# Performance work log

Hardware: AMD Instinct MI355X
Metric: run time of the kernel (lower is better)

Reference implementation:

```python
import jax, jax.numpy as jnp
import numpy as np
from functools import partial

NUM_CLASSES = 4
HEAD_OUTS = [4, 2, 1, 3, 2, 2]  # class, offset, z, size, yaw, vel -> sum 14
VOXEL = (0.1, 0.1)
PC_RANGE = (0.0, -39.68, -3.0, 100.0, 39.68, 1.0)
MIN_RADIUS = 2.0
BN_EPS = 1e-5


def setup_inputs() -> dict:
    key = jax.random.key(0)
    ks = jax.random.split(key, 12)
    B, C, H, W, N = 4, 256, 200, 200, 128
    spatial_features = jax.random.normal(ks[0], (B, C, H, W), jnp.float32)
    # gt boxes: x,y,z,w,l,h,yaw,cls,vx,vy ; coords chosen so grid idx in [0,200)
    x = jax.random.uniform(ks[1], (B, N), jnp.float32, 0.5, 19.5)
    y = jax.random.uniform(ks[2], (B, N), jnp.float32, -39.0, -20.0)
    z = jax.random.uniform(ks[3], (B, N), jnp.float32, -2.0, 0.0)
    dims = jax.random.uniform(ks[4], (B, N, 3), jnp.float32, 1.0, 4.0)
    yaw = jax.random.uniform(ks[5], (B, N), jnp.float32, -3.14159, 3.14159)
    cls = jax.random.randint(ks[6], (B, N), 0, NUM_CLASSES).astype(jnp.float32)
    vel = 0.1 * jax.random.normal(ks[7], (B, N, 2), jnp.float32)
    gt = jnp.concatenate([x[..., None], y[..., None], z[..., None], dims,
                          yaw[..., None], cls[..., None], vel], axis=-1)
    # zero out last 16 boxes per sample -> filtered by validity mask
    gt = gt.at[:, -16:, :].set(0.0)
    w1 = 0.05 * jax.random.normal(ks[8], (6, C, C, 3, 3), jnp.float32)
    bn_gamma = jnp.ones((6, C), jnp.float32)
    bn_beta = jnp.zeros((6, C), jnp.float32)
    bn_mean = 0.1 * jax.random.normal(ks[9], (6, C), jnp.float32)
    bn_var = jax.random.uniform(ks[10], (6, C), jnp.float32, 0.5, 1.5)
    w2 = 0.05 * jax.random.normal(ks[11], (14, C, 1, 1), jnp.float32)
    b2 = jnp.zeros((14,), jnp.float32)
    return {"spatial_features": spatial_features, "gt_boxes": gt, "w1": w1,
            "bn_gamma": bn_gamma, "bn_beta": bn_beta, "bn_mean": bn_mean,
            "bn_var": bn_var, "w2": w2, "b2": b2}


def _conv(x, w, pad):
    return jax.lax.conv_general_dilated(x, w, (1, 1), pad,
                                        dimension_numbers=("NCHW", "OIHW", "NCHW"))


def _heads(x, w1, g, b, m, v, w2, b2):
    outs, o = [], 0
    for i, nout in enumerate(HEAD_OUTS):
        h = _conv(x, w1[i], "SAME")  # [B,C,H,W]
        h = g[i][None, :, None, None] * (h - m[i][None, :, None, None]) \
            * jax.lax.rsqrt(v[i][None, :, None, None] + BN_EPS) + b[i][None, :, None, None]
        h = jax.nn.relu(h)
        outs.append(_conv(h, w2[o:o + nout], "VALID") + b2[o:o + nout][None, :, None, None])
        o += nout
    return jnp.concatenate(outs, axis=1)  # [B,14,H,W]


def _targets(gt, H, W):
    B, N = gt.shape[:2]
    x, y, z = gt[..., 0], gt[..., 1], gt[..., 2]
    bw, bl, bh = gt[..., 3], gt[..., 4], gt[..., 5]
    yaw = gt[..., 6]
    cls = jnp.clip(gt[..., 7].astype(jnp.int32), 0, NUM_CLASSES - 1)
    vel = gt[..., 8:10]
    valid = (jnp.abs(x) + jnp.abs(y) + jnp.abs(z)) > 0
    gx = (x - PC_RANGE[0]) / VOXEL[0]
    gy = (y - PC_RANGE[1]) / VOXEL[1]
    gxi = jnp.floor(gx).astype(jnp.int32)
    gyi = jnp.floor(gy).astype(jnp.int32)
    valid = valid & (gxi >= 0) & (gxi < W) & (gyi >= 0) & (gyi < H)
    xoff = gx - gxi.astype(gx.dtype)
    yoff = gy - gyi.astype(gy.dtype)
    # scalar targets scatter (invalid boxes dropped via out-of-range flat index)
    vals = jnp.stack([xoff, yoff, z, bw, bl, bh, jnp.sin(yaw), jnp.cos(yaw),
                      vel[..., 0], vel[..., 1], jnp.ones_like(x)], axis=-1)  # [B,N,11]
    bidx = jnp.broadcast_to(jnp.arange(B, dtype=jnp.int32)[:, None], (B, N))
    flat = bidx * (H * W) + gyi * W + gxi
    flat = jnp.where(valid, flat, B * H * W)  # out of range -> dropped
    scat = jnp.zeros((B * H * W, 11), jnp.float32)
    scat = scat.at[flat.reshape(-1)].set(vals.reshape(-1, 11), mode="drop")
    scalars = scat.reshape(B, H, W, 11).transpose(0, 3, 1, 2)  # [B,11,H,W]
    # gaussian heatmap: per-box splat, scatter-max into class channel
    sigma = jnp.maximum(jnp.sqrt(bw ** 2 + bl ** 2) / 2.0, MIN_RADIUS) / 3.0  # [B,N]
    xs = jnp.arange(W, dtype=jnp.float32)
    ys = jnp.arange(H, dtype=jnp.float32)
    d2 = (xs[None, None, None, :] - gxi[..., None, None].astype(jnp.float32)) ** 2 + \
         (ys[None, None, :, None] - gyi[..., None, None].astype(jnp.float32)) ** 2  # [B,N,H,W]
    gauss = jnp.exp(-d2 / (2.0 * sigma[..., None, None] ** 2))
    gauss = jnp.where(valid[..., None, None], gauss, 0.0)
    heat = jnp.zeros((B, NUM_CLASSES, H, W), jnp.float32)
    heat = heat.at[bidx, cls].max(gauss)
    return jnp.concatenate([heat, scalars], axis=1)  # [B,15,H,W]


def reference(spatial_features, gt_boxes, w1, bn_gamma, bn_beta, bn_mean, bn_var, w2, b2):
    H, W = spatial_features.shape[-2:]
    preds = _heads(spatial_features, w1, bn_gamma, bn_beta, bn_mean, bn_var, w2, b2)
    tgts = _targets(gt_boxes, H, W)
    return jnp.concatenate([preds, tgts], axis=1)  # [B,29,H,W]
```

## Files before the change

### kernel.cpp

```cpp
#include <hip/hip_runtime.h>

typedef __attribute__((ext_vector_type(8))) short short8;
typedef __attribute__((ext_vector_type(4))) float f32x4;
typedef __attribute__((ext_vector_type(4))) unsigned short us4;
typedef __attribute__((ext_vector_type(8))) unsigned short us8;

union FragU { short8 s; us4 h[2]; us8 u; };

__device__ __forceinline__ unsigned short f2bf(float f) {
  union { float f; unsigned int u; } v; v.f = f;
  unsigned int r = (v.u + 0x7fffu + ((v.u >> 16) & 1u)) >> 16;
  return (unsigned short)r;
}

typedef const __attribute__((address_space(1))) unsigned int* gas1_t;
typedef __attribute__((address_space(3))) unsigned int* las3_t;
__device__ __forceinline__ void glds16(const void* g, void* l) {
  __builtin_amdgcn_global_load_lds((gas1_t)g, (las3_t)l, 16, 0, 0);
}

__global__ void transpose_pad_k(const float* __restrict__ sf, unsigned short* __restrict__ Xtp) {
  __shared__ float tile[32][33];
  int b = blockIdx.z, c0 = blockIdx.y * 32, p0 = blockIdx.x * 32;
  int tx = threadIdx.x, ty = threadIdx.y;
#pragma unroll
  for (int i = 0; i < 4; ++i)
    tile[ty + i * 8][tx] = sf[((size_t)(b * 256 + c0 + ty + i * 8) * 40000) + p0 + tx];
  __syncthreads();
#pragma unroll
  for (int i = 0; i < 4; ++i) {
    int p = p0 + ty + i * 8;
    int y = p / 200, x = p - y * 200;
    size_t pf = (size_t)b * 40804 + (size_t)(y + 1) * 202 + (x + 1);
    Xtp[(pf << 8) + c0 + tx] = f2bf(tile[tx][ty + i * 8]);
  }
}

__global__ void border_zero_k(unsigned short* __restrict__ Xtp) {
  int t = blockIdx.x * 256 + threadIdx.x;
  if (t >= 4 * 804 * 32) return;
  int ch8 = t & 31;
  int rest = t >> 5;
  int p = rest % 804, b = rest / 804;
  int y, x;
  if (p < 202)      { y = 0;           x = p; }
  else if (p < 404) { y = 201;         x = p - 202; }
  else if (p < 604) { y = p - 404 + 1; x = 0; }
  else              { y = p - 604 + 1; x = 201; }
  size_t pf = (size_t)b * 40804 + (size_t)y * 202 + x;
  *(us8*)&Xtp[(pf << 8) + ch8 * 8] = (us8){0, 0, 0, 0, 0, 0, 0, 0};
}

__global__ void prep_w1f_k(const float* __restrict__ w1, const float* __restrict__ gamma,
                           const float* __restrict__ var, unsigned short* __restrict__ W1f) {
  int id = blockIdx.x * 256 + threadIdx.x;
  if (id >= 6 * 256 * 2304) return;
  int k = id % 2304;
  int rest = id / 2304;
  int oc = rest & 255, h = rest >> 8;
  int tap = k >> 8, c = k & 255;
  int hc = h * 256 + oc;
  float s = gamma[hc] * rsqrtf(var[hc] + 1e-5f);
  W1f[id] = f2bf(s * w1[(hc * 256 + c) * 9 + tap]);
}

__global__ __launch_bounds__(256, 2) void conv_head_v6_k(
    const unsigned short* __restrict__ Xtp, const unsigned short* __restrict__ W1f,
    const float* __restrict__ gamma, const float* __restrict__ beta,
    const float* __restrict__ mean, const float* __restrict__ var,
    const float* __restrict__ w2, const float* __restrict__ b2,
    float* __restrict__ out) {
  const int NOUT[6] = {4, 2, 1, 3, 2, 2};
  const int OFFS[6] = {0, 4, 6, 7, 10, 12};
  __shared__ __align__(16) char smem[73728];
  unsigned short* h_s = (unsigned short*)smem;

  int tid = threadIdx.x;
  int head = blockIdx.z, b = blockIdx.y;
  int p_loc = blockIdx.x * 128;
  int nout = NOUT[head], ooff = OFFS[head];

  int wid = tid >> 6, lane = tid & 63;
  int wm = wid >> 1, wn = wid & 1;
  int l15 = lane & 15, lhi = lane >> 4;

  int r0 = tid >> 2;
  int cbsw = (((tid & 3) ^ ((tid >> 3) & 3)) << 4);
  int pA0 = p_loc + r0;       if (pA0 > 39999) pA0 = 39999;
  int pA1 = p_loc + r0 + 64;  if (pA1 > 39999) pA1 = 39999;
  int ay0 = pA0 / 200, ax0 = pA0 - ay0 * 200;
  int ay1 = pA1 / 200, ax1 = pA1 - ay1 * 200;
  const char* xb = (const char*)Xtp + (size_t)b * 40804 * 512;
  const char* As0 = xb + (size_t)((ay0 + 1) * 202 + ax0 + 1) * 512 + cbsw;
  const char* As1 = xb + (size_t)((ay1 + 1) * 202 + ax1 + 1) * 512 + cbsw;

  const char* Bs0 = (const char*)W1f + (size_t)(head * 256 + r0) * 4608 + cbsw;
  const char* Bs1 = Bs0 + (size_t)64 * 4608;
  const char* Bs2 = Bs0 + (size_t)128 * 4608;
  const char* Bs3 = Bs0 + (size_t)192 * 4608;

  char* rA = smem;
  char* rB = smem + 24576;
  char* rC = smem + 49152;

  auto STAGE = [&](int kn, char* dst) {
    int tap = kn >> 3;
    int c0b = (kn & 7) << 6;
    int t3 = tap / 3;
    int doff = (t3 - 1) * 202 + (tap - t3 * 3 - 1);
    long ab = (long)doff * 512 + c0b;
    long bb = (long)kn * 64;
    glds16(As0 + ab, dst + wid * 1024);
    glds16(As1 + ab, dst + wid * 1024 + 4096);
    glds16(Bs0 + bb, dst + 8192 + wid * 1024);
    glds16(Bs1 + bb, dst + 8192 + wid * 1024 + 4096);
    glds16(Bs2 + bb, dst + 8192 + wid * 1024 + 8192);
    glds16(Bs3 + bb, dst + 8192 + wid * 1024 + 12288);
  };

  f32x4 acc[4][8];
#pragma unroll
  for (int mi = 0; mi < 4; ++mi)
#pragma unroll
    for (int ni = 0; ni < 8; ++ni) acc[mi][ni] = (f32x4){0.f, 0.f, 0.f, 0.f};

  STAGE(0, rA);
  STAGE(1, rB);

  int slotA = (lhi ^ ((l15 >> 1) & 3)) * 8;

  for (int kt = 0; kt < 72; ++kt) {
    if (kt < 71) asm volatile("s_waitcnt vmcnt(6)" ::: "memory");
    else         asm volatile("s_waitcnt vmcnt(0)" ::: "memory");
    __builtin_amdgcn_sched_barrier(0);
    __builtin_amdgcn_s_barrier();
    __builtin_amdgcn_sched_barrier(0);

    if (kt < 70) STAGE(kt + 2, rC);

    const unsigned short* A_sh = (const unsigned short*)rA;
    const unsigned short* B_sh = (const unsigned short*)(rA + 8192);
    short8 af[4], bfr[8];
#pragma unroll
    for (int mi = 0; mi < 4; ++mi) {
      FragU u;
      u.u = *(const us8*)&A_sh[(wm * 64 + mi * 16 + l15) * 32 + slotA];
      af[mi] = u.s;
    }
#pragma unroll
    for (int ni = 0; ni < 8; ++ni) {
      FragU u;
      u.u = *(const us8*)&B_sh[(wn * 128 + ni * 16 + l15) * 32 + slotA];
      bfr[ni] = u.s;
    }
    __builtin_amdgcn_s_setprio(1);
#pragma unroll
    for (int mi = 0; mi < 4; ++mi)
#pragma unroll
      for (int ni = 0; ni < 8; ++ni)
        acc[mi][ni] = __builtin_amdgcn_mfma_f32_16x16x32_bf16(af[mi], bfr[ni], acc[mi][ni], 0, 0, 0);
    __builtin_amdgcn_s_setprio(0);

    char* t = rA; rA = rB; rB = rC; rC = t;
  }

  {
    float tbr[8];
#pragma unroll
    for (int ni = 0; ni < 8; ++ni) {
      int hc = head * 256 + wn * 128 + ni * 16 + l15;
      float s = gamma[hc] * rsqrtf(var[hc] + 1e-5f);
      tbr[ni] = beta[hc] - s * mean[hc];
    }
#pragma unroll
    for (int mi = 0; mi < 4; ++mi)
#pragma unroll
      for (int ni = 0; ni < 8; ++ni)
#pragma unroll
        for (int r = 0; r < 4; ++r)
          acc[mi][ni][r] = fmaxf(acc[mi][ni][r] + tbr[ni], 0.f);
  }
  short8 wfr[8];
  {
    int jr = (l15 < nout) ? (ooff + l15) : 0;
    const float* wrow = w2 + jr * 256;
#pragma unroll
    for (int kc = 0; kc < 8; ++kc) {
      int koff = kc * 32 + lhi * 8;
      FragU u;
#pragma unroll
      for (int q = 0; q < 8; ++q) u.u[q] = f2bf(wrow[koff + q]);
      wfr[kc] = u.s;
    }
  }
  __syncthreads();
#pragma unroll
  for (int mi = 0; mi < 4; ++mi) {
#pragma unroll
    for (int ni = 0; ni < 8; ++ni) {
      int ocl = wn * 128 + ni * 16 + l15;
#pragma unroll
      for (int r = 0; r < 4; ++r) {
        int px = wm * 64 + mi * 16 + lhi * 4 + r;
        h_s[px * 264 + ocl] = f2bf(acc[mi][ni][r]);
      }
    }
  }
  __syncthreads();

#pragma unroll
  for (int g2 = 0; g2 < 2; ++g2) {
    int grp = wid * 2 + g2;
    float b2v = (l15 < nout) ? b2[ooff + l15] : 0.f;
    f32x4 oacc = (f32x4){0.f, 0.f, 0.f, 0.f};
#pragma unroll
    for (int kc = 0; kc < 8; ++kc) {
      int koff = kc * 32 + lhi * 8;
      FragU hu;
      hu.u = *(const us8*)&h_s[(grp * 16 + l15) * 264 + koff];
      oacc = __builtin_amdgcn_mfma_f32_16x16x32_bf16(hu.s, wfr[kc], oacc, 0, 0, 0);
    }
    if (l15 < nout) {
      float* dst = out + (size_t)(b * 29 + ooff + l15) * 40000;
#pragma unroll
      for (int r = 0; r < 4; ++r) {
        int px_g = p_loc + grp * 16 + lhi * 4 + r;
        if (px_g < 40000) dst[px_g] = oacc[r] + b2v;
      }
    }
  }
}

__global__ __launch_bounds__(512) void conv_head_nows_k(
    const float* __restrict__ sf, const float* __restrict__ w1,
    const float* __restrict__ gamma, const float* __restrict__ beta,
    const float* __restrict__ mean, const float* __restrict__ var,
    const float* __restrict__ w2, const float* __restrict__ b2,
    float* __restrict__ out) {
  const int NOUT[6] = {4, 2, 1, 3, 2, 2};
  const int OFFS[6] = {0, 4, 6, 7, 10, 12};
  __shared__ __align__(16) char smem[78080];
  unsigned short* A_s  = (unsigned short*)smem;
  unsigned short* B_s  = (unsigned short*)(smem + 9216);
  unsigned short* h_s  = (unsigned short*)smem;
  unsigned short* w2_s = (unsigned short*)(smem + 67584);
  float* tb_s          = (float*)(smem + 76032);
  float* s_s           = (float*)(smem + 77056);

  int tid = threadIdx.x;
  int head = blockIdx.z, b = blockIdx.y;
  int p_loc = blockIdx.x * 128;
  int nout = NOUT[head], ooff = OFFS[head];
  {
    int j = tid >> 5, c8 = (tid & 31) * 8;
    us8 t;
#pragma unroll
    for (int q = 0; q < 8; ++q)
      t[q] = (j < nout) ? f2bf(w2[(ooff + j) * 256 + c8 + q]) : (unsigned short)0;
    *(us8*)&w2_s[j * 264 + c8] = t;
  }
  if (tid < 256) {
    int hc = head * 256 + tid;
    float s = gamma[hc] * rsqrtf(var[hc] + 1e-5f);
    s_s[tid] = s;
    tb_s[tid] = beta[hc] - s * mean[hc];
  }
  __syncthreads();

  int wid = tid >> 6, lane = tid & 63;
  int wm = wid >> 2, wn = wid & 3;
  int l15 = lane & 15, lhi = lane >> 4;
  int cg = wid, mm = lane;
  int p0 = p_loc + mm, p1 = p0 + 64;
  int ay0 = p0 / 200, ax0 = p0 - ay0 * 200;
  int ay1 = p1 / 200, ax1 = p1 - ay1 * 200;
  const float* sfb = sf + (size_t)b * 256 * 40000;
  int oc = tid >> 1, half = tid & 1;
  const float* w1h = w1 + ((size_t)head * 256 + oc) * 2304;
  float sv = s_s[oc];

  f32x4 acc[4][4];
#pragma unroll
  for (int mi = 0; mi < 4; ++mi)
#pragma unroll
    for (int ni = 0; ni < 4; ++ni) acc[mi][ni] = (f32x4){0.f, 0.f, 0.f, 0.f};

  for (int kt = 0; kt < 72; ++kt) {
    int tap = kt >> 3;
    int c0 = (kt & 7) << 5;
    int t3 = tap / 3;
    int dy = t3 - 1, dx = tap - t3 * 3 - 1;
    {
      const float* src = sfb + (size_t)(c0 + cg * 4) * 40000;
      int yy = ay0 + dy, xx = ax0 + dx;
      us4 v = (us4){0, 0, 0, 0};
      if ((unsigned)yy < 200u && (unsigned)xx < 200u) {
        int pix = yy * 200 + xx;
        v[0] = f2bf(src[pix]);
        v[1] = f2bf(src[40000 + pix]);
        v[2] = f2bf(src[80000 + pix]);
        v[3] = f2bf(src[120000 + pix]);
      }
      *(us4*)&A_s[mm * 36 + cg * 4] = v;
      yy = ay1 + dy; xx = ax1 + dx;
      us4 w = (us4){0, 0, 0, 0};
      if ((unsigned)yy < 200u && (unsigned)xx < 200u) {
        int pix = yy * 200 + xx;
        w[0] = f2bf(src[pix]);
        w[1] = f2bf(src[40000 + pix]);
        w[2] = f2bf(src[80000 + pix]);
        w[3] = f2bf(src[120000 + pix]);
      }
      *(us4*)&A_s[(mm + 64) * 36 + cg * 4] = w;
    }
    {
      int kk = half * 16;
#pragma unroll
      for (int g = 0; g < 4; ++g) {
        us4 t;
#pragma unroll
        for (int q = 0; q < 4; ++q)
          t[q] = f2bf(sv * w1h[(c0 + kk + g * 4 + q) * 9 + tap]);
        *(us4*)&B_s[oc * 36 + kk + g * 4] = t;
      }
    }
    __syncthreads();
    short8 af[4], bfr[4];
#pragma unroll
    for (int mi = 0; mi < 4; ++mi) {
      int a = (wm * 64 + mi * 16 + l15) * 36 + lhi * 8;
      FragU u;
      u.h[0] = *(const us4*)&A_s[a];
      u.h[1] = *(const us4*)&A_s[a + 4];
      af[mi] = u.s;
    }
#pragma unroll
    for (int ni = 0; ni < 4; ++ni) {
      int a = (wn * 64 + ni * 16 + l15) * 36 + lhi * 8;
      FragU u;
      u.h[0] = *(const us4*)&B_s[a];
      u.h[1] = *(const us4*)&B_s[a + 4];
      bfr[ni] = u.s;
    }
#pragma unroll
    for (int mi = 0; mi < 4; ++mi)
#pragma unroll
      for (int ni = 0; ni < 4; ++ni)
        acc[mi][ni] = __builtin_amdgcn_mfma_f32_16x16x32_bf16(af[mi], bfr[ni], acc[mi][ni], 0, 0, 0);
    __syncthreads();
  }
#pragma unroll
  for (int mi = 0; mi < 4; ++mi) {
#pragma unroll
    for (int ni = 0; ni < 4; ++ni) {
      int ocl = wn * 64 + ni * 16 + l15;
      float tbv = tb_s[ocl];
#pragma unroll
      for (int r = 0; r < 4; ++r) {
        int px = wm * 64 + mi * 16 + lhi * 4 + r;
        float v = fmaxf(acc[mi][ni][r] + tbv, 0.f);
        h_s[px * 264 + ocl] = f2bf(v);
      }
    }
  }
  __syncthreads();
  {
    int j = l15;
    float b2v = (j < nout) ? b2[ooff + j] : 0.f;
    f32x4 oacc = (f32x4){0.f, 0.f, 0.f, 0.f};
#pragma unroll
    for (int kc = 0; kc < 8; ++kc) {
      int koff = kc * 32 + lhi * 8;
      FragU hu, wu;
      hu.u = *(const us8*)&h_s[(wid * 16 + l15) * 264 + koff];
      wu.u = *(const us8*)&w2_s[l15 * 264 + koff];
      oacc = __builtin_amdgcn_mfma_f32_16x16x32_bf16(hu.s, wu.s, oacc, 0, 0, 0);
    }
    if (j < nout) {
      float* dst = out + (size_t)(b * 29 + ooff + j) * 40000;
#pragma unroll
      for (int r = 0; r < 4; ++r) {
        int px_g = p_loc + wid * 16 + lhi * 4 + r;
        if (px_g < 40000) dst[px_g] = oacc[r] + b2v;
      }
    }
  }
}

__global__ void heat_k(const float* __restrict__ gt, float* __restrict__ out) {
  __shared__ float bx[128], by[128], binv[128];
  __shared__ int bcls[128];
  int b = blockIdx.y, tid = threadIdx.x;
  if (tid < 128) {
    const float* g = gt + (b * 128 + tid) * 10;
    float x = g[0], y = g[1], z = g[2];
    bool valid = fabsf(x) + fabsf(y) + fabsf(z) > 0.f;
    float gx = x / 0.1f;
    float gy = (y + 39.68f) / 0.1f;
    float fx = floorf(gx), fy = floorf(gy);
    int gxi = (int)fx, gyi = (int)fy;
    valid = valid && gxi >= 0 && gxi < 200 && gyi >= 0 && gyi < 200;
    float bw = g[3], bl = g[4];
    float sigma = fmaxf(sqrtf(bw * bw + bl * bl) * 0.5f, 2.0f) / 3.0f;
    binv[tid] = valid ? 1.f / (2.f * sigma * sigma) : -1.f;
    bx[tid] = fx;
    by[tid] = fy;
    bcls[tid] = min(max((int)g[7], 0), 3);
  }
  __syncthreads();
  int pid = blockIdx.x * 256 + tid;
  if (pid >= 40000) return;
  float py = (float)(pid / 200);
  float px = (float)(pid - (pid / 200) * 200);
  float h0 = 0.f, h1 = 0.f, h2 = 0.f, h3 = 0.f;
  for (int n = 0; n < 128; ++n) {
    float inv = binv[n];
    if (inv < 0.f) continue;
    float ddx = px - bx[n], ddy = py - by[n];
    float t = (ddx * ddx + ddy * ddy) * inv;
    if (t > 40.f) continue;
    float e = __expf(-t);
    int c = bcls[n];
    h0 = fmaxf(h0, c == 0 ? e : 0.f);
    h1 = fmaxf(h1, c == 1 ? e : 0.f);
    h2 = fmaxf(h2, c == 2 ? e : 0.f);
    h3 = fmaxf(h3, c == 3 ? e : 0.f);
  }
  int base = (b * 29 + 14) * 40000 + pid;
  out[base] = h0;
  out[base + 40000] = h1;
  out[base + 80000] = h2;
  out[base + 120000] = h3;
#pragma unroll
  for (int q = 0; q < 11; ++q) out[base + (4 + q) * 40000] = 0.f;
}

__global__ void scatter_k(const float* __restrict__ gt, float* __restrict__ out) {
  int b = threadIdx.x;
  if (b >= 4) return;
  for (int n = 0; n < 128; ++n) {
    const float* g = gt + (b * 128 + n) * 10;
    float x = g[0], y = g[1], z = g[2];
    if (!(fabsf(x) + fabsf(y) + fabsf(z) > 0.f)) continue;
    float gx = x / 0.1f;
    float gy = (y + 39.68f) / 0.1f;
    float fx = floorf(gx), fy = floorf(gy);
    int gxi = (int)fx, gyi = (int)fy;
    if (gxi < 0 || gxi >= 200 || gyi < 0 || gyi >= 200) continue;
    int base = (b * 29 + 18) * 40000 + gyi * 200 + gxi;
    out[base] = gx - fx;
    out[base + 1 * 40000] = gy - fy;
    out[base + 2 * 40000] = z;
    out[base + 3 * 40000] = g[3];
    out[base + 4 * 40000] = g[4];
    out[base + 5 * 40000] = g[5];
    out[base + 6 * 40000] = sinf(g[6]);
    out[base + 7 * 40000] = cosf(g[6]);
    out[base + 8 * 40000] = g[8];
    out[base + 9 * 40000] = g[9];
    out[base + 10 * 40000] = 1.f;
  }
}

extern "C" void kernel_launch(void* const* d_in, const int* in_sizes, int n_in,
                              void* d_out, int out_size, void* d_ws, size_t ws_size,
                              hipStream_t stream) {
  const float* sf    = (const float*)d_in[0];
  const float* gt    = (const float*)d_in[1];
  const float* w1    = (const float*)d_in[2];
  const float* gamma = (const float*)d_in[3];
  const float* beta  = (const float*)d_in[4];
  const float* mean  = (const float*)d_in[5];
  const float* var   = (const float*)d_in[6];
  const float* w2    = (const float*)d_in[7];
  const float* b2    = (const float*)d_in[8];
  float* out = (float*)d_out;
  char* ws = (char*)d_ws;

  const size_t W1F_BYTES = (size_t)6 * 256 * 2304 * 2;
  const size_t XTP_BYTES = (size_t)4 * 40804 * 256 * 2;
  unsigned short* W1f = (unsigned short*)ws;

  dim3 cgrid(313, 4, 6);
  if (ws_size >= W1F_BYTES + XTP_BYTES) {
    unsigned short* Xtp = (unsigned short*)(ws + W1F_BYTES);
    prep_w1f_k<<<(6 * 256 * 2304 + 255) / 256, 256, 0, stream>>>(w1, gamma, var, W1f);
    border_zero_k<<<(4 * 804 * 32 + 255) / 256, 256, 0, stream>>>(Xtp);
    transpose_pad_k<<<dim3(1250, 8, 4), dim3(32, 8), 0, stream>>>(sf, Xtp);
    conv_head_v6_k<<<cgrid, 256, 0, stream>>>(Xtp, W1f, gamma, beta, mean, var, w2, b2, out);
  } else {
    conv_head_nows_k<<<cgrid, 512, 0, stream>>>(sf, w1, gamma, beta, mean, var, w2, b2, out);
  }
  heat_k<<<dim3(157, 4), 256, 0, stream>>>(gt, out);
  scatter_k<<<1, 64, 0, stream>>>(gt, out);
}
```

Baseline: 1.211 ms.

## Switch conv head to double-buffered staging and fp32 scalar 1x1 epilogue

```diff
diff --git a/kernel.cpp b/kernel.cpp
--- a/kernel.cpp
+++ b/kernel.cpp
@@ -64,7 +64,7 @@
   W1f[id] = f2bf(s * w1[(hc * 256 + c) * 9 + tap]);
 }
 
-__global__ __launch_bounds__(256, 2) void conv_head_v6_k(
+__global__ __launch_bounds__(256, 2) void conv_head_v9_k(
     const unsigned short* __restrict__ Xtp, const unsigned short* __restrict__ W1f,
     const float* __restrict__ gamma, const float* __restrict__ beta,
     const float* __restrict__ mean, const float* __restrict__ var,
@@ -72,8 +72,7 @@
     float* __restrict__ out) {
   const int NOUT[6] = {4, 2, 1, 3, 2, 2};
   const int OFFS[6] = {0, 4, 6, 7, 10, 12};
-  __shared__ __align__(16) char smem[73728];
-  unsigned short* h_s = (unsigned short*)smem;
+  __shared__ __align__(16) char smem[49152];
 
   int tid = threadIdx.x;
   int head = blockIdx.z, b = blockIdx.y;
@@ -101,7 +100,6 @@
 
   char* rA = smem;
   char* rB = smem + 24576;
-  char* rC = smem + 49152;
 
   auto STAGE = [&](int kn, char* dst) {
     int tap = kn >> 3;
@@ -125,18 +123,16 @@
     for (int ni = 0; ni < 8; ++ni) acc[mi][ni] = (f32x4){0.f, 0.f, 0.f, 0.f};
 
   STAGE(0, rA);
-  STAGE(1, rB);
 
   int slotA = (lhi ^ ((l15 >> 1) & 3)) * 8;
 
   for (int kt = 0; kt < 72; ++kt) {
-    if (kt < 71) asm volatile("s_waitcnt vmcnt(6)" ::: "memory");
-    else         asm volatile("s_waitcnt vmcnt(0)" ::: "memory");
+    asm volatile("s_waitcnt vmcnt(0)" ::: "memory");
     __builtin_amdgcn_sched_barrier(0);
     __builtin_amdgcn_s_barrier();
     __builtin_amdgcn_sched_barrier(0);
 
-    if (kt < 70) STAGE(kt + 2, rC);
+    if (kt < 71) STAGE(kt + 1, rB);
 
     const unsigned short* A_sh = (const unsigned short*)rA;
     const unsigned short* B_sh = (const unsigned short*)(rA + 8192);
@@ -161,7 +157,7 @@
         acc[mi][ni] = __builtin_amdgcn_mfma_f32_16x16x32_bf16(af[mi], bfr[ni], acc[mi][ni], 0, 0, 0);
     __builtin_amdgcn_s_setprio(0);
 
-    char* t = rA; rA = rB; rB = rC; rC = t;
+    char* t = rA; rA = rB; rB = t;
   }
 
   {
@@ -180,52 +176,48 @@
         for (int r = 0; r < 4; ++r)
           acc[mi][ni][r] = fmaxf(acc[mi][ni][r] + tbr[ni], 0.f);
   }
-  short8 wfr[8];
-  {
-    int jr = (l15 < nout) ? (ooff + l15) : 0;
-    const float* wrow = w2 + jr * 256;
-#pragma unroll
-    for (int kc = 0; kc < 8; ++kc) {
-      int koff = kc * 32 + lhi * 8;
-      FragU u;
-#pragma unroll
-      for (int q = 0; q < 8; ++q) u.u[q] = f2bf(wrow[koff + q]);
-      wfr[kc] = u.s;
-    }
-  }
-  __syncthreads();
-#pragma unroll
-  for (int mi = 0; mi < 4; ++mi) {
-#pragma unroll
-    for (int ni = 0; ni < 8; ++ni) {
-      int ocl = wn * 128 + ni * 16 + l15;
-#pragma unroll
-      for (int r = 0; r < 4; ++r) {
-        int px = wm * 64 + mi * 16 + lhi * 4 + r;
-        h_s[px * 264 + ocl] = f2bf(acc[mi][ni][r]);
-      }
-    }
-  }
-  __syncthreads();
-
-#pragma unroll
-  for (int g2 = 0; g2 < 2; ++g2) {
-    int grp = wid * 2 + g2;
-    float b2v = (l15 < nout) ? b2[ooff + l15] : 0.f;
-    f32x4 oacc = (f32x4){0.f, 0.f, 0.f, 0.f};
-#pragma unroll
-    for (int kc = 0; kc < 8; ++kc) {
-      int koff = kc * 32 + lhi * 8;
-      FragU hu;
-      hu.u = *(const us8*)&h_s[(grp * 16 + l15) * 264 + koff];
-      oacc = __builtin_amdgcn_mfma_f32_16x16x32_bf16(hu.s, wfr[kc], oacc, 0, 0, 0);
-    }
-    if (l15 < nout) {
-      float* dst = out + (size_t)(b * 29 + ooff + l15) * 40000;
-#pragma unroll
-      for (int r = 0; r < 4; ++r) {
-        int px_g = p_loc + grp * 16 + lhi * 4 + r;
-        if (px_g < 40000) dst[px_g] = oacc[r] + b2v;
+
+  float* hcs = (float*)smem;
+#pragma unroll
+  for (int chunk = 0; chunk < 4; ++chunk) {
+    __syncthreads();
+    if (wm == (chunk >> 1)) {
+      int mi0 = (chunk & 1) * 2;
+#pragma unroll
+      for (int mi2 = 0; mi2 < 2; ++mi2) {
+#pragma unroll
+        for (int ni = 0; ni < 8; ++ni) {
+          int ocl = wn * 128 + ni * 16 + l15;
+#pragma unroll
+          for (int r = 0; r < 4; ++r)
+            hcs[(mi2 * 16 + lhi * 4 + r) * 264 + ocl] = acc[mi0 + mi2][ni][r];
+        }
+      }
+    }
+    __syncthreads();
+    {
+      int pxl = tid >> 3, ln = tid & 7;
+      float pj[4] = {0.f, 0.f, 0.f, 0.f};
+#pragma unroll
+      for (int i = 0; i < 32; ++i) {
+        float hv = hcs[pxl * 264 + ln + i * 8];
+#pragma unroll
+        for (int j = 0; j < 4; ++j)
+          if (j < nout) pj[j] += hv * w2[(ooff + j) * 256 + ln + i * 8];
+      }
+#pragma unroll
+      for (int j = 0; j < 4; ++j) {
+        float v = pj[j];
+        v += __shfl_xor(v, 1, 8);
+        v += __shfl_xor(v, 2, 8);
+        v += __shfl_xor(v, 4, 8);
+        pj[j] = v;
+      }
+      if (ln == 0) {
+        int px_g = p_loc + chunk * 32 + pxl;
+        if (px_g < 40000)
+          for (int j = 0; j < nout; ++j)
+            out[(size_t)(b * 29 + ooff + j) * 40000 + px_g] = pj[j] + b2[ooff + j];
       }
     }
   }
@@ -487,7 +479,7 @@
     prep_w1f_k<<<(6 * 256 * 2304 + 255) / 256, 256, 0, stream>>>(w1, gamma, var, W1f);
     border_zero_k<<<(4 * 804 * 32 + 255) / 256, 256, 0, stream>>>(Xtp);
     transpose_pad_k<<<dim3(1250, 8, 4), dim3(32, 8), 0, stream>>>(sf, Xtp);
-    conv_head_v6_k<<<cgrid, 256, 0, stream>>>(Xtp, W1f, gamma, beta, mean, var, w2, b2, out);
+    conv_head_v9_k<<<cgrid, 256, 0, stream>>>(Xtp, W1f, gamma, beta, mean, var, w2, b2, out);
   } else {
     conv_head_nows_k<<<cgrid, 512, 0, stream>>>(sf, w1, gamma, beta, mean, var, w2, b2, out);
   }
```

New measurement: 1.508 ms. +24.6%, slower.
